# Kernel optimization log

Measured on AMD Instinct MI355X. Metric: run time of the kernel, lower is better.

## Reference

```python
import jax, jax.numpy as jnp
import numpy as np

THRESH = 0.5
TAU = 0.5
GAMMA = 1.0
BETA = 0.9
A = 0.5
B = 0.5


def zif_spike(v):
    # ZIF surrogate: forward is hard threshold (v > 0).
    return (v > 0).astype(v.dtype)


def setup_inputs() -> dict:
    key = jax.random.key(0)
    x = jax.random.normal(key, (64, 8192, 100), dtype=jnp.float32)
    return {"x": x}


def reference(x):
    # x: [B, N, T]; scan over time with (mem, w) state kept per element.
    xt = jnp.moveaxis(x, 2, 0)  # [T, B, N]
    init_mem = jnp.zeros(xt.shape[1:], dtype=x.dtype)
    init_w = jnp.zeros(xt.shape[1:], dtype=x.dtype)

    def step(carry, x_t):
        mem, w = carry
        mem = mem * TAU + x_t - w
        spike = zif_spike(mem - THRESH)
        w = BETA * w + (1.0 - BETA) * (A * mem + B * spike)
        mem = mem - spike * THRESH  # soft reset
        return (mem, w), spike

    _, spikes = jax.lax.scan(step, (init_mem, init_w), xt)  # [T, B, N]
    return jnp.moveaxis(spikes, 0, 2)  # [B, N, T]
```

## Files before the change

kernel.cpp:

```cpp
#include <hip/hip_runtime.h>

#define T_STEPS 100
#define CHUNKS  25
#define ELEMS   128
#define TPB     128
#define ROW4    32

__device__ __forceinline__ int slot(int e, int c) {
    return e * ROW4 + (c ^ (e & 7));
}

__global__ __launch_bounds__(TPB) void lif_kernel(const float* __restrict__ x,
                                                  float* __restrict__ out) {
#pragma clang fp contract(off)
    __shared__ float4 tile[ELEMS * ROW4];

    const int tid = threadIdx.x;
    const size_t tile4 = (size_t)blockIdx.x * (ELEMS * CHUNKS);
    const float4* __restrict__ xb = (const float4*)x + tile4;
    float4* __restrict__ ob = (float4*)out + tile4;

    {
        int e = tid / 25;
        int c = tid - e * 25;
#pragma unroll
        for (int k = 0; k < CHUNKS; ++k) {
            float4 v = xb[k * TPB + tid];
            tile[slot(e, c)] = v;
            c += 3; e += 5;
            if (c >= CHUNKS) { c -= CHUNKS; e += 1; }
        }
    }
    __syncthreads();

    {
        float mem = 0.0f;
        float w = 0.0f;
#pragma unroll
        for (int c = 0; c < CHUNKS; ++c) {
            float4 xv4 = tile[slot(tid, c)];
            float xv[4] = {xv4.x, xv4.y, xv4.z, xv4.w};
            float sv[4];
#pragma unroll
            for (int j = 0; j < 4; ++j) {
                mem = (mem * 0.5f + xv[j]) - w;
                float spike = (mem - 0.5f) > 0.0f ? 1.0f : 0.0f;
                w = 0.9f * w + 0.1f * (0.5f * mem + 0.5f * spike);
                mem = mem - spike * 0.5f;
                sv[j] = spike;
            }
            float4 s4;
            s4.x = sv[0]; s4.y = sv[1]; s4.z = sv[2]; s4.w = sv[3];
            tile[slot(tid, c)] = s4;
        }
    }
    __syncthreads();

    {
        int e = tid / 25;
        int c = tid - e * 25;
#pragma unroll
        for (int k = 0; k < CHUNKS; ++k) {
            float4 s = tile[slot(e, c)];
            ob[k * TPB + tid] = s;
            c += 3; e += 5;
            if (c >= CHUNKS) { c -= CHUNKS; e += 1; }
        }
    }
}

extern "C" void kernel_launch(void* const* d_in, const int* in_sizes, int n_in,
                              void* d_out, int out_size, void* d_ws, size_t ws_size,
                              hipStream_t stream) {
    const float* x = (const float*)d_in[0];
    float* out = (float*)d_out;
    int n_elem = in_sizes[0] / T_STEPS;
    int grid = n_elem / ELEMS;

    lif_kernel<<<grid, TPB, 0, stream>>>(x, out);
}
```

Before: 350.8 us.

## Load input tile directly into LDS with global_load_lds and shrink blocks to one wave

Replaces the register-staged global-to-shared copy with the AMD global_load_lds builtin, so 16-byte chunks go straight from global memory into LDS without passing through VGPRs. To fit that builtin's layout rules, blocks shrink to a single 64-thread wave and the XOR-swizzled shared layout becomes a plain linear one. The linear layout, with a stride of 25 float4 per element, may cause LDS bank conflicts in the compute phase, and smaller blocks change occupancy and scheduling. The store-back phase is also simplified to linear indexing.

Result: no change. 344.4 us (-1.8%).

```diff
diff --git a/kernel.cpp b/kernel.cpp
--- a/kernel.cpp
+++ b/kernel.cpp
@@ -2,34 +2,28 @@
 
 #define T_STEPS 100
 #define CHUNKS  25
-#define ELEMS   128
-#define TPB     128
-#define ROW4    32
+#define TPB     64
+#define ELEMS   64
 
-__device__ __forceinline__ int slot(int e, int c) {
-    return e * ROW4 + (c ^ (e & 7));
-}
+typedef const __attribute__((address_space(1))) unsigned int g_u32;
+typedef __attribute__((address_space(3))) unsigned int l_u32;
 
 __global__ __launch_bounds__(TPB) void lif_kernel(const float* __restrict__ x,
                                                   float* __restrict__ out) {
 #pragma clang fp contract(off)
-    __shared__ float4 tile[ELEMS * ROW4];
+    __shared__ float4 tile[ELEMS * CHUNKS];
 
-    const int tid = threadIdx.x;
+    const int lane = threadIdx.x;
     const size_t tile4 = (size_t)blockIdx.x * (ELEMS * CHUNKS);
     const float4* __restrict__ xb = (const float4*)x + tile4;
     float4* __restrict__ ob = (float4*)out + tile4;
 
-    {
-        int e = tid / 25;
-        int c = tid - e * 25;
 #pragma unroll
-        for (int k = 0; k < CHUNKS; ++k) {
-            float4 v = xb[k * TPB + tid];
-            tile[slot(e, c)] = v;
-            c += 3; e += 5;
-            if (c >= CHUNKS) { c -= CHUNKS; e += 1; }
-        }
+    for (int k = 0; k < CHUNKS; ++k) {
+        __builtin_amdgcn_global_load_lds(
+            (g_u32*)(xb + k * TPB + lane),
+            (l_u32*)&tile[k * TPB],
+            16, 0, 0);
     }
     __syncthreads();
 
@@ -38,7 +32,7 @@
         float w = 0.0f;
 #pragma unroll
         for (int c = 0; c < CHUNKS; ++c) {
-            float4 xv4 = tile[slot(tid, c)];
+            float4 xv4 = tile[lane * CHUNKS + c];
             float xv[4] = {xv4.x, xv4.y, xv4.z, xv4.w};
             float sv[4];
 #pragma unroll
@@ -51,21 +45,15 @@
             }
             float4 s4;
             s4.x = sv[0]; s4.y = sv[1]; s4.z = sv[2]; s4.w = sv[3];
-            tile[slot(tid, c)] = s4;
+            tile[lane * CHUNKS + c] = s4;
         }
     }
     __syncthreads();
 
-    {
-        int e = tid / 25;
-        int c = tid - e * 25;
 #pragma unroll
-        for (int k = 0; k < CHUNKS; ++k) {
-            float4 s = tile[slot(e, c)];
-            ob[k * TPB + tid] = s;
-            c += 3; e += 5;
-            if (c >= CHUNKS) { c -= CHUNKS; e += 1; }
-        }
+    for (int k = 0; k < CHUNKS; ++k) {
+        float4 s = tile[k * TPB + lane];
+        ob[k * TPB + lane] = s;
     }
 }
 
```
